# Kernel tuning notes

Hardware: AMD Instinct MI355X
Metric: run time of the kernel (lower is better)

The kernel has to match this reference:

```python
import jax, jax.numpy as jnp
import numpy as np
import math

D = 1024      # d_model
K = 64        # k_eigenstates
H = 4         # n_heads
KH = K // H   # eigenstates per head
MLP = 4 * D
B, T = 4, 4096


def setup_inputs() -> dict:
    key = jax.random.key(0)
    ks = jax.random.split(key, 16)
    rn = lambda k, shape, s: (jax.random.normal(k, shape, jnp.float32) * s)
    inp = {
        "x": rn(ks[0], (B, T, D), 1.0),
        "W_in": rn(ks[1], (2 * K, D), 1.0 / math.sqrt(D)),
        "log_decay": jax.random.uniform(ks[2], (K,), jnp.float32, -3.0, -0.1),
        "frequency": jnp.linspace(0.0, 2 * math.pi * (1 - 1.0 / K), K, dtype=jnp.float32),
        "W_sel": rn(ks[3], (2 * K, D), 0.01 / math.sqrt(D)),
        "b_sel": jnp.zeros((2 * K,), jnp.float32),
        "R": jnp.eye(KH, dtype=jnp.float32)[None] + 0.01 * rn(ks[4], (H, KH, KH), 1.0 / math.sqrt(KH)),
        "W_out": rn(ks[5], (D, 2 * K), 1.0 / math.sqrt(2 * K)),
        "W_g": rn(ks[6], (D, D), 1.0 / math.sqrt(D)),
        "b_g": jnp.full((D,), -2.0, jnp.float32),
        "g1": jnp.ones((D,), jnp.float32),
        "be1": jnp.zeros((D,), jnp.float32),
        "g2": jnp.ones((D,), jnp.float32),
        "be2": jnp.zeros((D,), jnp.float32),
        "W1": rn(ks[7], (MLP, D), 1.0 / math.sqrt(D)),
        "b1": jnp.zeros((MLP,), jnp.float32),
        "W2": rn(ks[8], (D, MLP), 1.0 / math.sqrt(MLP)),
        "b2": jnp.zeros((D,), jnp.float32),
    }
    return inp


def _ln(x, g, b):
    m = jnp.mean(x, axis=-1, keepdims=True)
    v = jnp.mean(jnp.square(x - m), axis=-1, keepdims=True)
    return (x - m) * jax.lax.rsqrt(v + 1e-5) * g + b


def _scan_combine(e1, e2):
    a1, b1 = e1
    a2, b2 = e2
    return a1 * a2, a2 * b1 + b2


def reference(x, W_in, log_decay, frequency, W_sel, b_sel, R, W_out, W_g, b_g,
              g1, be1, g2, be2, W1, b1, W2, b2):
    Bsz, Ts, Dm = x.shape
    residual = x
    x_norm = _ln(x, g1, be1)

    beta = x_norm @ W_in.T                      # [B,T,2K]
    beta_r, beta_i = jnp.split(beta, 2, axis=-1)

    delta = x_norm @ W_sel.T + b_sel            # selective modulation
    d_dec, d_fr = jnp.split(delta, 2, axis=-1)
    mag = jax.nn.sigmoid(log_decay + 0.1 * jnp.tanh(d_dec))   # [B,T,K]
    freq = frequency + 0.05 * jnp.tanh(d_fr)

    a = jax.lax.complex(mag * jnp.cos(freq), mag * jnp.sin(freq))  # lambda_t
    bc = jax.lax.complex(beta_r, beta_i)
    # inclusive prefix scan of c_t = a_t * c_{t-1} + b_t
    _, c = jax.lax.associative_scan(_scan_combine, (a, bc), axis=1)
    c_r, c_i = c.real, c.imag                   # [B,T,K]

    nH, Kh = R.shape[0], R.shape[1]
    c_r = jnp.einsum('hjk,bthk->bthj', R, c_r.reshape(Bsz, Ts, nH, Kh)).reshape(Bsz, Ts, -1)
    c_i = jnp.einsum('hjk,bthk->bthj', R, c_i.reshape(Bsz, Ts, nH, Kh)).reshape(Bsz, Ts, -1)

    h = jnp.concatenate([c_r, c_i], axis=-1) @ W_out.T
    gate = jax.nn.sigmoid(x_norm @ W_g.T + b_g)
    x = residual + gate * h

    x2 = _ln(x, g2, be2)
    x = x + (jax.nn.silu(x2 @ W1.T + b1) @ W2.T + b2)
    return x
```

## Files before the change

kernel.cpp:

```cpp
#include <hip/hip_runtime.h>
#include <math.h>

typedef __bf16 bf16_t;
typedef __attribute__((ext_vector_type(8))) __bf16 bf16x8;
typedef __attribute__((ext_vector_type(4))) float f32x4;

#define DMODEL 1024
#define NROWS  16384
#define SEQLEN 4096

static __device__ __forceinline__ float sigmoidf_(float v) { return 1.f / (1.f + __expf(-v)); }

#define GLOAD16(gsrc, ldst) __builtin_amdgcn_global_load_lds(                     \
    (const __attribute__((address_space(1))) void*)(gsrc),                        \
    (__attribute__((address_space(3))) void*)(ldst), 16, 0, 0)

__global__ __launch_bounds__(256) void ln_fused_kernel(const float* __restrict__ x,
                                                       const float* __restrict__ g,
                                                       const float* __restrict__ b,
                                                       bf16_t* __restrict__ out) {
  int row = blockIdx.x;
  int tid = threadIdx.x;
  const float4* xr = (const float4*)(x + (size_t)row * DMODEL);
  float4 v = xr[tid];
  float s  = v.x + v.y + v.z + v.w;
  float s2 = v.x*v.x + v.y*v.y + v.z*v.z + v.w*v.w;
  #pragma unroll
  for (int off = 32; off > 0; off >>= 1) {
    s  += __shfl_down(s, off);
    s2 += __shfl_down(s2, off);
  }
  __shared__ float sh[4], sh2[4];
  int lane = tid & 63, wid = tid >> 6;
  if (lane == 0) { sh[wid] = s; sh2[wid] = s2; }
  __syncthreads();
  s  = sh[0] + sh[1] + sh[2] + sh[3];
  s2 = sh2[0] + sh2[1] + sh2[2] + sh2[3];
  float m = s * (1.f / DMODEL);
  float var = fmaxf(s2 * (1.f / DMODEL) - m * m, 0.f);
  float rs = rsqrtf(var + 1e-5f);
  float4 gv = *(const float4*)&g[tid * 4];
  float4 bv = *(const float4*)&b[tid * 4];
  union { bf16_t h[4]; float2 f2; } u;
  u.h[0] = (bf16_t)((v.x - m) * rs * gv.x + bv.x);
  u.h[1] = (bf16_t)((v.y - m) * rs * gv.y + bv.y);
  u.h[2] = (bf16_t)((v.z - m) * rs * gv.z + bv.z);
  u.h[3] = (bf16_t)((v.w - m) * rs * gv.w + bv.w);
  *(float2*)&out[(size_t)row * DMODEL + tid * 4] = u.f2;
}

__global__ __launch_bounds__(256) void f32_to_bf16_kernel(const float* __restrict__ in,
                                                          bf16_t* __restrict__ out, int n) {
  int idx = (blockIdx.x * 256 + threadIdx.x) * 4;
  if (idx >= n) return;
  float4 v = *(const float4*)&in[idx];
  union { bf16_t h[4]; float2 f2; } u;
  u.h[0] = (bf16_t)v.x; u.h[1] = (bf16_t)v.y; u.h[2] = (bf16_t)v.z; u.h[3] = (bf16_t)v.w;
  *(float2*)&out[idx] = u.f2;
}

template<int EPI>
__global__ __launch_bounds__(512, 4) void gemmB_kernel(
    const bf16_t* __restrict__ A, int lda,
    const bf16_t* __restrict__ B, int ldb, int K, int nx,
    const float* __restrict__ bias,
    const float* __restrict__ res,
    const bf16_t* __restrict__ auxb,
    float* __restrict__ outf, bf16_t* __restrict__ outb, int ldout) {
  __shared__ __align__(128) bf16_t Asm[128 * 64];
  __shared__ __align__(128) bf16_t Bsm[256 * 64];
  const int nwg = gridDim.x;
  const int bid = blockIdx.x;
  const int lid = (bid & 7) * (nwg >> 3) + (bid >> 3);
  const int n0 = (lid % nx) * 256;
  const int r0 = (lid / nx) * 128;

  const int tid = threadIdx.x;
  const int lane = tid & 63;
  const int w = tid >> 6;
  const int wr = w >> 2, wc = w & 3;
  const int fr = lane & 15;
  const int q16 = (lane >> 4) * 16;
  const int swz = (fr & 7) << 4;
  const int trow = tid >> 3;
  const int scolb = ((tid & 7) ^ (trow & 7)) << 4;

  const size_t lda_b = (size_t)lda * 2;
  const size_t ldb_b = (size_t)ldb * 2;
  const char* Ab = (const char*)A;
  const char* Bb = (const char*)B;
  char* lA = (char*)Asm;
  char* lB = (char*)Bsm;

  f32x4 acc[4][4];
  #pragma unroll
  for (int m = 0; m < 4; ++m)
    #pragma unroll
    for (int n = 0; n < 4; ++n) acc[m][n] = (f32x4){0.f, 0.f, 0.f, 0.f};

  for (int kt = 0; kt < K; kt += 64) {
    const char* sa = Ab + (size_t)(r0 + trow) * lda_b + kt * 2 + scolb;
    GLOAD16(sa, lA + tid * 16);
    GLOAD16(sa + 64 * lda_b, lA + 8192 + tid * 16);
    const char* sb = Bb + (size_t)(n0 + trow) * ldb_b + kt * 2 + scolb;
    GLOAD16(sb, lB + tid * 16);
    GLOAD16(sb + 64 * ldb_b,  lB + 8192  + tid * 16);
    GLOAD16(sb + 128 * ldb_b, lB + 16384 + tid * 16);
    GLOAD16(sb + 192 * ldb_b, lB + 24576 + tid * 16);
    __syncthreads();
    #pragma unroll
    for (int kh = 0; kh < 2; ++kh) {
      bf16x8 af[4], bv[4];
      #pragma unroll
      for (int m = 0; m < 4; ++m)
        af[m] = *(const bf16x8*)(lA + (wr * 64 + m * 16 + fr) * 128 + ((kh * 64 + q16) ^ swz));
      #pragma unroll
      for (int n = 0; n < 4; ++n)
        bv[n] = *(const bf16x8*)(lB + (wc * 64 + n * 16 + fr) * 128 + ((kh * 64 + q16) ^ swz));
      #pragma unroll
      for (int m = 0; m < 4; ++m)
        #pragma unroll
        for (int n = 0; n < 4; ++n)
          acc[m][n] = __builtin_amdgcn_mfma_f32_16x16x32_bf16(af[m], bv[n], acc[m][n], 0, 0, 0);
    }
    __syncthreads();
  }

  const int rbase = (lane >> 4) * 4;
  #pragma unroll
  for (int mf = 0; mf < 4; ++mf) {
    #pragma unroll
    for (int n = 0; n < 4; ++n) {
      int row = r0 + wr * 64 + mf * 16 + rbase;
      int col = n0 + wc * 64 + n * 16 + fr;
      f32x4 v = acc[mf][n];
      #pragma unroll
      for (int j = 0; j < 4; ++j) {
        int r = row + j;
        float val = v[j];
        if (EPI == 0) {
          outf[(size_t)r * ldout + col] = val;
        } else if (EPI == 1) {
          float t2 = val + bias[col];
          t2 = t2 * sigmoidf_(t2);
          outb[(size_t)r * ldout + col] = (bf16_t)t2;
        } else if (EPI == 2) {
          outf[(size_t)r * ldout + col] = res[(size_t)r * 1024 + col] + bias[col] + val;
        } else if (EPI == 3) {
          outf[(size_t)r * ldout + col] += val;
        } else if (EPI == 4) {
          size_t idx = (size_t)r * 1024 + col;
          outf[idx] = res[idx] + sigmoidf_(val + bias[col]) * (float)auxb[idx];
        } else {
          outb[(size_t)r * ldout + col] = (bf16_t)val;
        }
      }
    }
  }
}

template<int EPI>
__global__ __launch_bounds__(256) void gemm_bf16_kernel(
    const bf16_t* __restrict__ A, int lda,
    const bf16_t* __restrict__ B, int ldb, int K, int nx,
    float* __restrict__ outf, int ldout) {
  __shared__ __align__(16) bf16_t As[128 * 32];
  __shared__ __align__(16) bf16_t Bs[128 * 32];
  const int nwg = gridDim.x;
  const int bid = blockIdx.x;
  const int lid = (bid & 7) * (nwg >> 3) + (bid >> 3);
  const int n0 = (lid % nx) * 128;
  const int r0 = (lid / nx) * 128;

  const int tid = threadIdx.x;
  const int lane = tid & 63;
  const int w = tid >> 6;
  const int wr = w >> 1, wc = w & 1;
  const int srow0 = tid >> 2;
  const int srow1 = 64 + (tid >> 2);
  const int skk = (tid & 3) * 8;
  const int fr = lane & 15;
  const int ko = (lane >> 4) * 8;

  f32x4 acc[4][4];
  #pragma unroll
  for (int m = 0; m < 4; ++m)
    #pragma unroll
    for (int n = 0; n < 4; ++n) acc[m][n] = (f32x4){0.f, 0.f, 0.f, 0.f};

  for (int k0 = 0; k0 < K; k0 += 32) {
    GLOAD16(A + (size_t)(r0 + srow0) * lda + k0 + skk, (char*)As + w * 1024);
    GLOAD16(A + (size_t)(r0 + srow1) * lda + k0 + skk, (char*)As + 4096 + w * 1024);
    GLOAD16(B + (size_t)(n0 + srow0) * ldb + k0 + skk, (char*)Bs + w * 1024);
    GLOAD16(B + (size_t)(n0 + srow1) * ldb + k0 + skk, (char*)Bs + 4096 + w * 1024);
    __syncthreads();
    bf16x8 af[4], bfr[4];
    #pragma unroll
    for (int m = 0; m < 4; ++m)
      af[m] = *(const bf16x8*)&As[(wr * 64 + m * 16 + fr) * 32 + ko];
    #pragma unroll
    for (int n = 0; n < 4; ++n)
      bfr[n] = *(const bf16x8*)&Bs[(wc * 64 + n * 16 + fr) * 32 + ko];
    #pragma unroll
    for (int m = 0; m < 4; ++m)
      #pragma unroll
      for (int n = 0; n < 4; ++n)
        acc[m][n] = __builtin_amdgcn_mfma_f32_16x16x32_bf16(af[m], bfr[n], acc[m][n], 0, 0, 0);
    __syncthreads();
  }

  const int rbase = (lane >> 4) * 4;
  #pragma unroll
  for (int m = 0; m < 4; ++m) {
    #pragma unroll
    for (int n = 0; n < 4; ++n) {
      int row = r0 + wr * 64 + m * 16 + rbase;
      int col = n0 + wc * 64 + n * 16 + fr;
      f32x4 v = acc[m][n];
      #pragma unroll
      for (int j = 0; j < 4; ++j)
        outf[(size_t)(row + j) * ldout + col] = v[j];
    }
  }
}

__global__ __launch_bounds__(256) void ew_ab_kernel(
    const float* __restrict__ bd, const float* __restrict__ b_sel,
    const float* __restrict__ log_decay, const float* __restrict__ frequency,
    float* __restrict__ a_r, float* __restrict__ a_i,
    float* __restrict__ b_r, float* __restrict__ b_i) {
  __shared__ float T[32][257];
  int bb = blockIdx.x >> 7;
  int t0 = (blockIdx.x & 127) << 5;
  int tid = threadIdx.x;
  #pragma unroll
  for (int p = 0; p < 32; ++p) {
    int idx = tid + p * 256;
    int tt = idx >> 8, j = idx & 255;
    T[tt][j] = bd[((size_t)bb * 4096 + t0 + tt) * 256 + j];
  }
  __syncthreads();
  #pragma unroll
  for (int p = 0; p < 8; ++p) {
    int idx = tid + p * 256;
    int tt = idx & 31, k = idx >> 5;
    float br_ = T[tt][k];
    float bi_ = T[tt][64 + k];
    float dd = T[tt][128 + k] + b_sel[k];
    float df = T[tt][192 + k] + b_sel[64 + k];
    float mag = sigmoidf_(log_decay[k] + 0.1f * tanhf(dd));
    float fr = frequency[k] + 0.05f * tanhf(df);
    float ar_ = mag * cosf(fr), ai_ = mag * sinf(fr);
    size_t o = ((size_t)bb * 64 + k) * 4096 + t0 + tt;
    a_r[o] = ar_; a_i[o] = ai_; b_r[o] = br_; b_i[o] = bi_;
  }
}

__global__ __launch_bounds__(256) void scan_kernel(
    const float* __restrict__ a_r, const float* __restrict__ a_i,
    const float* b_r, const float* b_i,
    float* c_r, float* c_i) {
  int seq = blockIdx.x;
  size_t base = (size_t)seq * SEQLEN;
  int tid = threadIdx.x;
  int t0 = tid * 16;
  float Ar = 1.f, Ai = 0.f, Br = 0.f, Bi = 0.f;
  #pragma unroll
  for (int s = 0; s < 16; ++s) {
    size_t t = base + t0 + s;
    float ar = a_r[t], ai = a_i[t], br = b_r[t], bi = b_i[t];
    float nBr = ar * Br - ai * Bi + br;
    float nBi = ar * Bi + ai * Br + bi;
    Br = nBr; Bi = nBi;
    float nAr = ar * Ar - ai * Ai;
    float nAi = ar * Ai + ai * Ar;
    Ar = nAr; Ai = nAi;
  }
  __shared__ float sAr[256], sAi[256], sBr[256], sBi[256];
  sAr[tid] = Ar; sAi[tid] = Ai; sBr[tid] = Br; sBi[tid] = Bi;
  for (int off = 1; off < 256; off <<= 1) {
    __syncthreads();
    float pAr = 0.f, pAi = 0.f, pBr = 0.f, pBi = 0.f;
    if (tid >= off) { pAr = sAr[tid - off]; pAi = sAi[tid - off]; pBr = sBr[tid - off]; pBi = sBi[tid - off]; }
    __syncthreads();
    if (tid >= off) {
      float cAr = sAr[tid], cAi = sAi[tid], cBr = sBr[tid], cBi = sBi[tid];
      float nBr = cAr * pBr - cAi * pBi + cBr;
      float nBi = cAr * pBi + cAi * pBr + cBi;
      float nAr = cAr * pAr - cAi * pAi;
      float nAi = cAr * pAi + cAi * pAr;
      sAr[tid] = nAr; sAi[tid] = nAi; sBr[tid] = nBr; sBi[tid] = nBi;
    }
  }
  __syncthreads();
  float cr = (tid > 0) ? sBr[tid - 1] : 0.f;
  float ci = (tid > 0) ? sBi[tid - 1] : 0.f;
  #pragma unroll
  for (int s = 0; s < 16; ++s) {
    size_t t = base + t0 + s;
    float ar = a_r[t], ai = a_i[t], br = b_r[t], bi = b_i[t];
    float nr = ar * cr - ai * ci + br;
    float ni = ar * ci + ai * cr + bi;
    cr = nr; ci = ni;
    c_r[t] = cr; c_i[t] = ci;
  }
}

__global__ __launch_bounds__(256) void transpose_cc_kernel(
    const float* __restrict__ c_r, const float* __restrict__ c_i,
    bf16_t* __restrict__ cc) {
  __shared__ float Tr[64][65];
  __shared__ float Ti[64][65];
  int t0 = blockIdx.x * 64;
  int bb = blockIdx.y;
  int tid = threadIdx.x;
  int tt = tid & 63;
  int q = tid >> 6;
  #pragma unroll
  for (int p = 0; p < 16; ++p) {
    int k = p * 4 + q;
    size_t src = ((size_t)bb * 64 + k) * 4096 + t0 + tt;
    Tr[tt][k] = c_r[src];
    Ti[tt][k] = c_i[src];
  }
  __syncthreads();
  #pragma unroll
  for (int p = 0; p < 16; ++p) {
    int tt2 = p * 4 + q;
    int k = tid & 63;
    size_t row = (size_t)bb * 4096 + t0 + tt2;
    cc[row * 128 + k] = (bf16_t)Tr[tt2][k];
    cc[row * 128 + 64 + k] = (bf16_t)Ti[tt2][k];
  }
}

__global__ __launch_bounds__(256) void weff_kernel(const float* __restrict__ W_out,
                                                   const float* __restrict__ R,
                                                   bf16_t* __restrict__ Weff) {
  int idx = blockIdx.x * 256 + threadIdx.x;
  int d = idx >> 7, col = idx & 127;
  int k = col & 63, h = k >> 4, kk = k & 15;
  int off = (col < 64) ? 0 : 64;
  float s = 0.f;
  #pragma unroll
  for (int j = 0; j < 16; ++j)
    s += W_out[d * 128 + off + h * 16 + j] * R[h * 256 + j * 16 + kk];
  Weff[idx] = (bf16_t)s;
}

extern "C" void kernel_launch(void* const* d_in, const int* in_sizes, int n_in,
                              void* d_out, int out_size, void* d_ws, size_t ws_size,
                              hipStream_t stream) {
  (void)in_sizes; (void)n_in; (void)out_size;
  const float* x         = (const float*)d_in[0];
  const float* W_in      = (const float*)d_in[1];
  const float* log_decay = (const float*)d_in[2];
  const float* frequency = (const float*)d_in[3];
  const float* W_sel     = (const float*)d_in[4];
  const float* b_sel     = (const float*)d_in[5];
  const float* R         = (const float*)d_in[6];
  const float* W_out     = (const float*)d_in[7];
  const float* W_g       = (const float*)d_in[8];
  const float* b_g       = (const float*)d_in[9];
  const float* g1        = (const float*)d_in[10];
  const float* be1       = (const float*)d_in[11];
  const float* g2        = (const float*)d_in[12];
  const float* be2       = (const float*)d_in[13];
  const float* W1        = (const float*)d_in[14];
  const float* b1        = (const float*)d_in[15];
  const float* W2        = (const float*)d_in[16];
  const float* b2        = (const float*)d_in[17];
  float* out = (float*)d_out;
  float* ws  = (float*)d_ws;

  const size_t M1 = (size_t)1 << 20;
  const bool full = ws_size >= (size_t)62 * M1 * sizeof(float);

  float* bd   = ws;
  float* xmid = ws;
  float* a_r  = ws + 16 * M1;
  float* a_i  = ws + 20 * M1;
  float* b_rr = ws + 24 * M1;
  float* b_ii = ws + 28 * M1;
  bf16_t* hbufb = (bf16_t*)(ws + 16 * M1);
  bf16_t* mid = (bf16_t*)(ws + 16 * M1);
  size_t wx = full ? 48 * M1 : 32 * M1;
  size_t wc_off = full ? 56 * M1 : 40 * M1;
  size_t wb = full ? 57 * M1 : 41 * M1;
  bf16_t* xn  = (bf16_t*)(ws + wx);
  bf16_t* cc  = (bf16_t*)(ws + wc_off);
  bf16_t* Wbd = (bf16_t*)(ws + wb);
  bf16_t* Wgb = (bf16_t*)(ws + wb + (128 << 10));
  bf16_t* W1b = (bf16_t*)(ws + wb + (640 << 10));
  bf16_t* W2b = (bf16_t*)(ws + wb + 2 * M1 + (640 << 10));
  bf16_t* Wef = (bf16_t*)(ws + wb + 4 * M1 + (640 << 10));

  dim3 blk(256);
  dim3 blk512(512);

  ln_fused_kernel<<<NROWS, blk, 0, stream>>>(x, g1, be1, xn);

  f32_to_bf16_kernel<<<128, blk, 0, stream>>>(W_in, Wbd, 128 * 1024);
  f32_to_bf16_kernel<<<128, blk, 0, stream>>>(W_sel, Wbd + 128 * 1024, 128 * 1024);
  f32_to_bf16_kernel<<<1024, blk, 0, stream>>>(W_g, Wgb, 1024 * 1024);
  f32_to_bf16_kernel<<<4096, blk, 0, stream>>>(W1, W1b, 4 * 1024 * 1024);
  f32_to_bf16_kernel<<<4096, blk, 0, stream>>>(W2, W2b, 4 * 1024 * 1024);
  weff_kernel<<<512, blk, 0, stream>>>(W_out, R, Wef);

  gemm_bf16_kernel<0><<<256, blk, 0, stream>>>(xn, 1024, Wbd, 1024, 1024, 2, bd, 256);

  ew_ab_kernel<<<512, blk, 0, stream>>>(bd, b_sel, log_decay, frequency, a_r, a_i, b_rr, b_ii);
  scan_kernel<<<256, blk, 0, stream>>>(a_r, a_i, b_rr, b_ii, b_rr, b_ii);
  transpose_cc_kernel<<<dim3(64, 4), blk, 0, stream>>>(b_rr, b_ii, cc);

  gemmB_kernel<5><<<512, blk512, 0, stream>>>(
      cc, 128, Wef, 128, 128, 4, nullptr, nullptr, nullptr, nullptr, hbufb, 1024);

  gemmB_kernel<4><<<512, blk512, 0, stream>>>(
      xn, 1024, Wgb, 1024, 1024, 4, b_g, x, hbufb, xmid, nullptr, 1024);

  ln_fused_kernel<<<NROWS, blk, 0, stream>>>(xmid, g2, be2, xn);

  if (full) {
    gemmB_kernel<1><<<2048, blk512, 0, stream>>>(
        xn, 1024, W1b, 1024, 1024, 16, b1, nullptr, nullptr, nullptr, mid, 4096);
    gemmB_kernel<2><<<512, blk512, 0, stream>>>(
        mid, 4096, W2b, 4096, 4096, 4, b2, xmid, nullptr, out, nullptr, 1024);
  } else {
    for (int h = 0; h < 2; ++h) {
      gemmB_kernel<1><<<1024, blk512, 0, stream>>>(
          xn, 1024, W1b + (size_t)h * 2048 * 1024, 1024, 1024, 8,
          b1 + h * 2048, nullptr, nullptr, nullptr, mid, 2048);
      if (h == 0) {
        gemmB_kernel<2><<<512, blk512, 0, stream>>>(
            mid, 2048, W2b, 4096, 2048, 4, b2, xmid, nullptr, out, nullptr, 1024);
      } else {
        gemmB_kernel<3><<<512, blk512, 0, stream>>>(
            mid, 2048, W2b + 2048, 4096, 2048, 4, nullptr, nullptr, nullptr, out, nullptr, 1024);
      }
    }
  }
}
```

Before: 476.7 us.

## Double-buffer LDS in main GEMM with 32-wide K tiles

Replaces the single-buffered 64-wide K-tile loop in the main bf16 GEMM with a double-buffered loop over 32-wide K tiles. The next tile's global-to-LDS load is issued before computing on the current one, which removes one barrier per iteration and overlaps memory with MFMA work. The XOR swizzle is dropped because each LDS row is now 64 bytes, which may bring back bank conflicts on the fragment reads. Each iteration also has half as many MFMAs to hide latency behind.

```diff
diff --git a/kernel.cpp b/kernel.cpp
--- a/kernel.cpp
+++ b/kernel.cpp
@@ -60,15 +60,14 @@
 }
 
 template<int EPI>
-__global__ __launch_bounds__(512, 4) void gemmB_kernel(
+__global__ __launch_bounds__(512, 4) void gemmC_kernel(
     const bf16_t* __restrict__ A, int lda,
     const bf16_t* __restrict__ B, int ldb, int K, int nx,
     const float* __restrict__ bias,
     const float* __restrict__ res,
     const bf16_t* __restrict__ auxb,
     float* __restrict__ outf, bf16_t* __restrict__ outb, int ldout) {
-  __shared__ __align__(128) bf16_t Asm[128 * 64];
-  __shared__ __align__(128) bf16_t Bsm[256 * 64];
+  __shared__ __align__(128) char ldsp[49152];
   const int nwg = gridDim.x;
   const int bid = blockIdx.x;
   const int lid = (bid & 7) * (nwg >> 3) + (bid >> 3);
@@ -81,16 +80,13 @@
   const int wr = w >> 2, wc = w & 3;
   const int fr = lane & 15;
   const int q16 = (lane >> 4) * 16;
-  const int swz = (fr & 7) << 4;
-  const int trow = tid >> 3;
-  const int scolb = ((tid & 7) ^ (trow & 7)) << 4;
+  const int tr4 = tid >> 2;
+  const int sl = (tid & 3) * 16;
 
   const size_t lda_b = (size_t)lda * 2;
   const size_t ldb_b = (size_t)ldb * 2;
   const char* Ab = (const char*)A;
   const char* Bb = (const char*)B;
-  char* lA = (char*)Asm;
-  char* lB = (char*)Bsm;
 
   f32x4 acc[4][4];
   #pragma unroll
@@ -98,32 +94,37 @@
     #pragma unroll
     for (int n = 0; n < 4; ++n) acc[m][n] = (f32x4){0.f, 0.f, 0.f, 0.f};
 
-  for (int kt = 0; kt < K; kt += 64) {
-    const char* sa = Ab + (size_t)(r0 + trow) * lda_b + kt * 2 + scolb;
-    GLOAD16(sa, lA + tid * 16);
-    GLOAD16(sa + 64 * lda_b, lA + 8192 + tid * 16);
-    const char* sb = Bb + (size_t)(n0 + trow) * ldb_b + kt * 2 + scolb;
-    GLOAD16(sb, lB + tid * 16);
-    GLOAD16(sb + 64 * ldb_b,  lB + 8192  + tid * 16);
-    GLOAD16(sb + 128 * ldb_b, lB + 16384 + tid * 16);
-    GLOAD16(sb + 192 * ldb_b, lB + 24576 + tid * 16);
-    __syncthreads();
-    #pragma unroll
-    for (int kh = 0; kh < 2; ++kh) {
-      bf16x8 af[4], bv[4];
-      #pragma unroll
-      for (int m = 0; m < 4; ++m)
-        af[m] = *(const bf16x8*)(lA + (wr * 64 + m * 16 + fr) * 128 + ((kh * 64 + q16) ^ swz));
+  auto stage = [&](int d, int kt) {
+    const char* sa = Ab + (size_t)(r0 + tr4) * lda_b + kt * 2 + sl;
+    GLOAD16(sa, ldsp + d * 8192 + tid * 16);
+    const char* sb = Bb + (size_t)(n0 + tr4) * ldb_b + kt * 2 + sl;
+    GLOAD16(sb, ldsp + 16384 + d * 16384 + tid * 16);
+    GLOAD16(sb + 128 * ldb_b, ldsp + 16384 + d * 16384 + 8192 + tid * 16);
+  };
+  auto compute = [&](int d) {
+    bf16x8 af[4], bv[4];
+    #pragma unroll
+    for (int m = 0; m < 4; ++m)
+      af[m] = *(const bf16x8*)(ldsp + d * 8192 + (wr * 64 + m * 16 + fr) * 64 + q16);
+    #pragma unroll
+    for (int n = 0; n < 4; ++n)
+      bv[n] = *(const bf16x8*)(ldsp + 16384 + d * 16384 + (wc * 64 + n * 16 + fr) * 64 + q16);
+    #pragma unroll
+    for (int m = 0; m < 4; ++m)
       #pragma unroll
       for (int n = 0; n < 4; ++n)
-        bv[n] = *(const bf16x8*)(lB + (wc * 64 + n * 16 + fr) * 128 + ((kh * 64 + q16) ^ swz));
-      #pragma unroll
-      for (int m = 0; m < 4; ++m)
-        #pragma unroll
-        for (int n = 0; n < 4; ++n)
-          acc[m][n] = __builtin_amdgcn_mfma_f32_16x16x32_bf16(af[m], bv[n], acc[m][n], 0, 0, 0);
-    }
+        acc[m][n] = __builtin_amdgcn_mfma_f32_16x16x32_bf16(af[m], bv[n], acc[m][n], 0, 0, 0);
+  };
+
+  const int nt = K >> 5;
+  stage(0, 0);
+  __syncthreads();
+  int d = 0;
+  for (int t = 0; t < nt; ++t) {
+    if (t + 1 < nt) stage(d ^ 1, (t + 1) << 5);
+    compute(d);
     __syncthreads();
+    d ^= 1;
   }
 
   const int rbase = (lane >> 4) * 4;
@@ -413,29 +414,29 @@
   scan_kernel<<<256, blk, 0, stream>>>(a_r, a_i, b_rr, b_ii, b_rr, b_ii);
   transpose_cc_kernel<<<dim3(64, 4), blk, 0, stream>>>(b_rr, b_ii, cc);
 
-  gemmB_kernel<5><<<512, blk512, 0, stream>>>(
+  gemmC_kernel<5><<<512, blk512, 0, stream>>>(
       cc, 128, Wef, 128, 128, 4, nullptr, nullptr, nullptr, nullptr, hbufb, 1024);
 
-  gemmB_kernel<4><<<512, blk512, 0, stream>>>(
+  gemmC_kernel<4><<<512, blk512, 0, stream>>>(
       xn, 1024, Wgb, 1024, 1024, 4, b_g, x, hbufb, xmid, nullptr, 1024);
 
   ln_fused_kernel<<<NROWS, blk, 0, stream>>>(xmid, g2, be2, xn);
 
   if (full) {
-    gemmB_kernel<1><<<2048, blk512, 0, stream>>>(
+    gemmC_kernel<1><<<2048, blk512, 0, stream>>>(
         xn, 1024, W1b, 1024, 1024, 16, b1, nullptr, nullptr, nullptr, mid, 4096);
-    gemmB_kernel<2><<<512, blk512, 0, stream>>>(
+    gemmC_kernel<2><<<512, blk512, 0, stream>>>(
         mid, 4096, W2b, 4096, 4096, 4, b2, xmid, nullptr, out, nullptr, 1024);
   } else {
     for (int h = 0; h < 2; ++h) {
-      gemmB_kernel<1><<<1024, blk512, 0, stream>>>(
+      gemmC_kernel<1><<<1024, blk512, 0, stream>>>(
           xn, 1024, W1b + (size_t)h * 2048 * 1024, 1024, 1024, 8,
           b1 + h * 2048, nullptr, nullptr, nullptr, mid, 2048);
       if (h == 0) {
-        gemmB_kernel<2><<<512, blk512, 0, stream>>>(
+        gemmC_kernel<2><<<512, blk512, 0, stream>>>(
             mid, 2048, W2b, 4096, 2048, 4, b2, xmid, nullptr, out, nullptr, 1024);
       } else {
-        gemmB_kernel<3><<<512, blk512, 0, stream>>>(
+        gemmC_kernel<3><<<512, blk512, 0, stream>>>(
             mid, 2048, W2b + 2048, 4096, 2048, 4, nullptr, nullptr, nullptr, out, nullptr, 1024);
       }
     }
```

After: 517.5 us. +8.6%, slower.

## Replace 512-thread GEMM with 256-thread 256x128 tile, K-step 32 kernel

Applied to the files above, without the earlier changes.

Swaps the main bf16 MFMA GEMM for a variant using 256 threads, a 256x128 output tile (rows x cols), and a 32-wide K step with a 24KB shared buffer and a new XOR swizzle. Each wave now computes a 128x64 sub-tile with 8x4 accumulators, loading each A fragment once per m and reusing the B fragments across all m. The aim is higher register-level reuse and smaller LDS use so more workgroups fit per CU. In exchange there are twice as many K iterations and barriers, and more accumulator registers per thread.

```diff
diff --git a/kernel.cpp b/kernel.cpp
--- a/kernel.cpp
+++ b/kernel.cpp
@@ -60,78 +60,71 @@
 }
 
 template<int EPI>
-__global__ __launch_bounds__(512, 4) void gemmB_kernel(
+__global__ __launch_bounds__(256, 3) void gemmD_kernel(
     const bf16_t* __restrict__ A, int lda,
     const bf16_t* __restrict__ B, int ldb, int K, int nx,
     const float* __restrict__ bias,
     const float* __restrict__ res,
     const bf16_t* __restrict__ auxb,
     float* __restrict__ outf, bf16_t* __restrict__ outb, int ldout) {
-  __shared__ __align__(128) bf16_t Asm[128 * 64];
-  __shared__ __align__(128) bf16_t Bsm[256 * 64];
+  __shared__ __align__(128) char ldsp[24576];
   const int nwg = gridDim.x;
   const int bid = blockIdx.x;
   const int lid = (bid & 7) * (nwg >> 3) + (bid >> 3);
-  const int n0 = (lid % nx) * 256;
-  const int r0 = (lid / nx) * 128;
+  const int n0 = (lid % nx) * 128;
+  const int r0 = (lid / nx) * 256;
 
   const int tid = threadIdx.x;
   const int lane = tid & 63;
   const int w = tid >> 6;
-  const int wr = w >> 2, wc = w & 3;
+  const int wr = w >> 1, wc = w & 1;
   const int fr = lane & 15;
   const int q16 = (lane >> 4) * 16;
-  const int swz = (fr & 7) << 4;
-  const int trow = tid >> 3;
-  const int scolb = ((tid & 7) ^ (trow & 7)) << 4;
+  const int rdcol = q16 ^ (((fr >> 1) & 3) << 4);
+  const int trow = tid >> 2;
+  const int scolb = (((tid & 3) ^ ((trow >> 1) & 3)) << 4);
 
   const size_t lda_b = (size_t)lda * 2;
   const size_t ldb_b = (size_t)ldb * 2;
   const char* Ab = (const char*)A;
   const char* Bb = (const char*)B;
-  char* lA = (char*)Asm;
-  char* lB = (char*)Bsm;
-
-  f32x4 acc[4][4];
-  #pragma unroll
-  for (int m = 0; m < 4; ++m)
+
+  f32x4 acc[8][4];
+  #pragma unroll
+  for (int m = 0; m < 8; ++m)
     #pragma unroll
     for (int n = 0; n < 4; ++n) acc[m][n] = (f32x4){0.f, 0.f, 0.f, 0.f};
 
-  for (int kt = 0; kt < K; kt += 64) {
+  for (int kt = 0; kt < K; kt += 32) {
     const char* sa = Ab + (size_t)(r0 + trow) * lda_b + kt * 2 + scolb;
-    GLOAD16(sa, lA + tid * 16);
-    GLOAD16(sa + 64 * lda_b, lA + 8192 + tid * 16);
+    GLOAD16(sa,               ldsp +         tid * 16);
+    GLOAD16(sa +  64 * lda_b, ldsp +  4096 + tid * 16);
+    GLOAD16(sa + 128 * lda_b, ldsp +  8192 + tid * 16);
+    GLOAD16(sa + 192 * lda_b, ldsp + 12288 + tid * 16);
     const char* sb = Bb + (size_t)(n0 + trow) * ldb_b + kt * 2 + scolb;
-    GLOAD16(sb, lB + tid * 16);
-    GLOAD16(sb + 64 * ldb_b,  lB + 8192  + tid * 16);
-    GLOAD16(sb + 128 * ldb_b, lB + 16384 + tid * 16);
-    GLOAD16(sb + 192 * ldb_b, lB + 24576 + tid * 16);
-    __syncthreads();
-    #pragma unroll
-    for (int kh = 0; kh < 2; ++kh) {
-      bf16x8 af[4], bv[4];
-      #pragma unroll
-      for (int m = 0; m < 4; ++m)
-        af[m] = *(const bf16x8*)(lA + (wr * 64 + m * 16 + fr) * 128 + ((kh * 64 + q16) ^ swz));
+    GLOAD16(sb,               ldsp + 16384 + tid * 16);
+    GLOAD16(sb +  64 * ldb_b, ldsp + 20480 + tid * 16);
+    __syncthreads();
+    bf16x8 bv[4];
+    #pragma unroll
+    for (int n = 0; n < 4; ++n)
+      bv[n] = *(const bf16x8*)(ldsp + 16384 + (wc * 64 + n * 16 + fr) * 64 + rdcol);
+    #pragma unroll
+    for (int m = 0; m < 8; ++m) {
+      bf16x8 af = *(const bf16x8*)(ldsp + (wr * 128 + m * 16 + fr) * 64 + rdcol);
       #pragma unroll
       for (int n = 0; n < 4; ++n)
-        bv[n] = *(const bf16x8*)(lB + (wc * 64 + n * 16 + fr) * 128 + ((kh * 64 + q16) ^ swz));
-      #pragma unroll
-      for (int m = 0; m < 4; ++m)
-        #pragma unroll
-        for (int n = 0; n < 4; ++n)
-          acc[m][n] = __builtin_amdgcn_mfma_f32_16x16x32_bf16(af[m], bv[n], acc[m][n], 0, 0, 0);
+        acc[m][n] = __builtin_amdgcn_mfma_f32_16x16x32_bf16(af, bv[n], acc[m][n], 0, 0, 0);
     }
     __syncthreads();
   }
 
   const int rbase = (lane >> 4) * 4;
   #pragma unroll
-  for (int mf = 0; mf < 4; ++mf) {
+  for (int mf = 0; mf < 8; ++mf) {
     #pragma unroll
     for (int n = 0; n < 4; ++n) {
-      int row = r0 + wr * 64 + mf * 16 + rbase;
+      int row = r0 + wr * 128 + mf * 16 + rbase;
       int col = n0 + wc * 64 + n * 16 + fr;
       f32x4 v = acc[mf][n];
       #pragma unroll
@@ -396,7 +389,6 @@
   bf16_t* Wef = (bf16_t*)(ws + wb + 4 * M1 + (640 << 10));
 
   dim3 blk(256);
-  dim3 blk512(512);
 
   ln_fused_kernel<<<NROWS, blk, 0, stream>>>(x, g1, be1, xn);
 
@@ -413,30 +405,30 @@
   scan_kernel<<<256, blk, 0, stream>>>(a_r, a_i, b_rr, b_ii, b_rr, b_ii);
   transpose_cc_kernel<<<dim3(64, 4), blk, 0, stream>>>(b_rr, b_ii, cc);
 
-  gemmB_kernel<5><<<512, blk512, 0, stream>>>(
-      cc, 128, Wef, 128, 128, 4, nullptr, nullptr, nullptr, nullptr, hbufb, 1024);
-
-  gemmB_kernel<4><<<512, blk512, 0, stream>>>(
-      xn, 1024, Wgb, 1024, 1024, 4, b_g, x, hbufb, xmid, nullptr, 1024);
+  gemmD_kernel<5><<<512, blk, 0, stream>>>(
+      cc, 128, Wef, 128, 128, 8, nullptr, nullptr, nullptr, nullptr, hbufb, 1024);
+
+  gemmD_kernel<4><<<512, blk, 0, stream>>>(
+      xn, 1024, Wgb, 1024, 1024, 8, b_g, x, hbufb, xmid, nullptr, 1024);
 
   ln_fused_kernel<<<NROWS, blk, 0, stream>>>(xmid, g2, be2, xn);
 
   if (full) {
-    gemmB_kernel<1><<<2048, blk512, 0, stream>>>(
-        xn, 1024, W1b, 1024, 1024, 16, b1, nullptr, nullptr, nullptr, mid, 4096);
-    gemmB_kernel<2><<<512, blk512, 0, stream>>>(
-        mid, 4096, W2b, 4096, 4096, 4, b2, xmid, nullptr, out, nullptr, 1024);
+    gemmD_kernel<1><<<2048, blk, 0, stream>>>(
+        xn, 1024, W1b, 1024, 1024, 32, b1, nullptr, nullptr, nullptr, mid, 4096);
+    gemmD_kernel<2><<<512, blk, 0, stream>>>(
+        mid, 4096, W2b, 4096, 4096, 8, b2, xmid, nullptr, out, nullptr, 1024);
   } else {
     for (int h = 0; h < 2; ++h) {
-      gemmB_kernel<1><<<1024, blk512, 0, stream>>>(
-          xn, 1024, W1b + (size_t)h * 2048 * 1024, 1024, 1024, 8,
+      gemmD_kernel<1><<<1024, blk, 0, stream>>>(
+          xn, 1024, W1b + (size_t)h * 2048 * 1024, 1024, 1024, 16,
           b1 + h * 2048, nullptr, nullptr, nullptr, mid, 2048);
       if (h == 0) {
-        gemmB_kernel<2><<<512, blk512, 0, stream>>>(
-            mid, 2048, W2b, 4096, 2048, 4, b2, xmid, nullptr, out, nullptr, 1024);
+        gemmD_kernel<2><<<512, blk, 0, stream>>>(
+            mid, 2048, W2b, 4096, 2048, 8, b2, xmid, nullptr, out, nullptr, 1024);
       } else {
-        gemmB_kernel<3><<<512, blk512, 0, stream>>>(
-            mid, 2048, W2b + 2048, 4096, 2048, 4, nullptr, nullptr, nullptr, out, nullptr, 1024);
+        gemmD_kernel<3><<<512, blk, 0, stream>>>(
+            mid, 2048, W2b + 2048, 4096, 2048, 8, nullptr, nullptr, nullptr, out, nullptr, 1024);
       }
     }
   }
```

Result: slower. 575.3 us (+20.7%).

## Fuse gate computation into scan, transpose beta GEMM, store residual stream in bf16

Applied to the files above, without the earlier changes.

The element-wise decay/frequency kernel is merged into the scan kernel. The projection GEMM is swapped to emit a transposed [256 x 16384] layout so the scan reads contiguous per-channel vectors, and it computes gates with fast tanh/sincos. The intermediate residual xmid is now stored as bf16, with a new bf16-input LayerNorm, to cut memory traffic in the second half. This removes the a/b round-trip buffers and one launch, at the cost of lower precision in the residual carried to the final output.

```diff
diff --git a/kernel.cpp b/kernel.cpp
--- a/kernel.cpp
+++ b/kernel.cpp
@@ -3,6 +3,7 @@
 
 typedef __bf16 bf16_t;
 typedef __attribute__((ext_vector_type(8))) __bf16 bf16x8;
+typedef __attribute__((ext_vector_type(4))) __bf16 bf16x4;
 typedef __attribute__((ext_vector_type(4))) float f32x4;
 
 #define DMODEL 1024
@@ -10,6 +11,11 @@
 #define SEQLEN 4096
 
 static __device__ __forceinline__ float sigmoidf_(float v) { return 1.f / (1.f + __expf(-v)); }
+static __device__ __forceinline__ float tanhf_(float v) {
+  v = fminf(fmaxf(v, -15.f), 15.f);
+  float e = __expf(-2.f * v);
+  return (1.f - e) / (1.f + e);
+}
 
 #define GLOAD16(gsrc, ldst) __builtin_amdgcn_global_load_lds(                     \
     (const __attribute__((address_space(1))) void*)(gsrc),                        \
@@ -49,6 +55,40 @@
   *(float2*)&out[(size_t)row * DMODEL + tid * 4] = u.f2;
 }
 
+__global__ __launch_bounds__(256) void ln_fused_bf16_kernel(const bf16_t* __restrict__ x,
+                                                            const float* __restrict__ g,
+                                                            const float* __restrict__ b,
+                                                            bf16_t* __restrict__ out) {
+  int row = blockIdx.x;
+  int tid = threadIdx.x;
+  bf16x4 hv = *(const bf16x4*)(x + (size_t)row * DMODEL + tid * 4);
+  float v0 = (float)hv[0], v1 = (float)hv[1], v2 = (float)hv[2], v3 = (float)hv[3];
+  float s  = v0 + v1 + v2 + v3;
+  float s2 = v0*v0 + v1*v1 + v2*v2 + v3*v3;
+  #pragma unroll
+  for (int off = 32; off > 0; off >>= 1) {
+    s  += __shfl_down(s, off);
+    s2 += __shfl_down(s2, off);
+  }
+  __shared__ float sh[4], sh2[4];
+  int lane = tid & 63, wid = tid >> 6;
+  if (lane == 0) { sh[wid] = s; sh2[wid] = s2; }
+  __syncthreads();
+  s  = sh[0] + sh[1] + sh[2] + sh[3];
+  s2 = sh2[0] + sh2[1] + sh2[2] + sh2[3];
+  float m = s * (1.f / DMODEL);
+  float var = fmaxf(s2 * (1.f / DMODEL) - m * m, 0.f);
+  float rs = rsqrtf(var + 1e-5f);
+  float4 gv = *(const float4*)&g[tid * 4];
+  float4 bv = *(const float4*)&b[tid * 4];
+  union { bf16_t h[4]; float2 f2; } u;
+  u.h[0] = (bf16_t)((v0 - m) * rs * gv.x + bv.x);
+  u.h[1] = (bf16_t)((v1 - m) * rs * gv.y + bv.y);
+  u.h[2] = (bf16_t)((v2 - m) * rs * gv.z + bv.z);
+  u.h[3] = (bf16_t)((v3 - m) * rs * gv.w + bv.w);
+  *(float2*)&out[(size_t)row * DMODEL + tid * 4] = u.f2;
+}
+
 __global__ __launch_bounds__(256) void f32_to_bf16_kernel(const float* __restrict__ in,
                                                           bf16_t* __restrict__ out, int n) {
   int idx = (blockIdx.x * 256 + threadIdx.x) * 4;
@@ -64,7 +104,8 @@
     const bf16_t* __restrict__ A, int lda,
     const bf16_t* __restrict__ B, int ldb, int K, int nx,
     const float* __restrict__ bias,
-    const float* __restrict__ res,
+    const float* __restrict__ resf,
+    const bf16_t* __restrict__ resb,
     const bf16_t* __restrict__ auxb,
     float* __restrict__ outf, bf16_t* __restrict__ outb, int ldout) {
   __shared__ __align__(128) bf16_t Asm[128 * 64];
@@ -145,12 +186,13 @@
           t2 = t2 * sigmoidf_(t2);
           outb[(size_t)r * ldout + col] = (bf16_t)t2;
         } else if (EPI == 2) {
-          outf[(size_t)r * ldout + col] = res[(size_t)r * 1024 + col] + bias[col] + val;
+          outf[(size_t)r * ldout + col] =
+              (float)resb[(size_t)r * 1024 + col] + bias[col] + val;
         } else if (EPI == 3) {
           outf[(size_t)r * ldout + col] += val;
         } else if (EPI == 4) {
           size_t idx = (size_t)r * 1024 + col;
-          outf[idx] = res[idx] + sigmoidf_(val + bias[col]) * (float)auxb[idx];
+          outb[idx] = (bf16_t)(resf[idx] + sigmoidf_(val + bias[col]) * (float)auxb[idx]);
         } else {
           outb[(size_t)r * ldout + col] = (bf16_t)val;
         }
@@ -224,58 +266,46 @@
   }
 }
 
-__global__ __launch_bounds__(256) void ew_ab_kernel(
-    const float* __restrict__ bd, const float* __restrict__ b_sel,
+__global__ __launch_bounds__(256) void scan_fused_kernel(
+    const float* __restrict__ bdt,
     const float* __restrict__ log_decay, const float* __restrict__ frequency,
-    float* __restrict__ a_r, float* __restrict__ a_i,
-    float* __restrict__ b_r, float* __restrict__ b_i) {
-  __shared__ float T[32][257];
-  int bb = blockIdx.x >> 7;
-  int t0 = (blockIdx.x & 127) << 5;
+    const float* __restrict__ b_sel,
+    float* __restrict__ c_r, float* __restrict__ c_i) {
+  int seq = blockIdx.x;
+  int bb = seq >> 6, k = seq & 63;
   int tid = threadIdx.x;
-  #pragma unroll
-  for (int p = 0; p < 32; ++p) {
-    int idx = tid + p * 256;
-    int tt = idx >> 8, j = idx & 255;
-    T[tt][j] = bd[((size_t)bb * 4096 + t0 + tt) * 256 + j];
-  }
-  __syncthreads();
-  #pragma unroll
-  for (int p = 0; p < 8; ++p) {
-    int idx = tid + p * 256;
-    int tt = idx & 31, k = idx >> 5;
-    float br_ = T[tt][k];
-    float bi_ = T[tt][64 + k];
-    float dd = T[tt][128 + k] + b_sel[k];
-    float df = T[tt][192 + k] + b_sel[64 + k];
-    float mag = sigmoidf_(log_decay[k] + 0.1f * tanhf(dd));
-    float fr = frequency[k] + 0.05f * tanhf(df);
-    float ar_ = mag * cosf(fr), ai_ = mag * sinf(fr);
-    size_t o = ((size_t)bb * 64 + k) * 4096 + t0 + tt;
-    a_r[o] = ar_; a_i[o] = ai_; b_r[o] = br_; b_i[o] = bi_;
-  }
-}
-
-__global__ __launch_bounds__(256) void scan_kernel(
-    const float* __restrict__ a_r, const float* __restrict__ a_i,
-    const float* b_r, const float* b_i,
-    float* c_r, float* c_i) {
-  int seq = blockIdx.x;
-  size_t base = (size_t)seq * SEQLEN;
-  int tid = threadIdx.x;
-  int t0 = tid * 16;
+  size_t col = (size_t)bb * 4096 + tid * 16;
+  const f32x4* pbr = (const f32x4*)(bdt + (size_t)k * 16384 + col);
+  const f32x4* pbi = (const f32x4*)(bdt + (size_t)(64 + k) * 16384 + col);
+  const f32x4* pdd = (const f32x4*)(bdt + (size_t)(128 + k) * 16384 + col);
+  const f32x4* pdf = (const f32x4*)(bdt + (size_t)(192 + k) * 16384 + col);
+  const float ld = log_decay[k], fq = frequency[k];
+  const float bsd = b_sel[k], bsf = b_sel[64 + k];
+
+  float arv[16], aiv[16], brv[16], biv[16];
   float Ar = 1.f, Ai = 0.f, Br = 0.f, Bi = 0.f;
   #pragma unroll
-  for (int s = 0; s < 16; ++s) {
-    size_t t = base + t0 + s;
-    float ar = a_r[t], ai = a_i[t], br = b_r[t], bi = b_i[t];
-    float nBr = ar * Br - ai * Bi + br;
-    float nBi = ar * Bi + ai * Br + bi;
-    Br = nBr; Bi = nBi;
-    float nAr = ar * Ar - ai * Ai;
-    float nAi = ar * Ai + ai * Ar;
-    Ar = nAr; Ai = nAi;
-  }
+  for (int g = 0; g < 4; ++g) {
+    f32x4 vbr = pbr[g], vbi = pbi[g], vdd = pdd[g], vdf = pdf[g];
+    #pragma unroll
+    for (int j = 0; j < 4; ++j) {
+      int s = g * 4 + j;
+      float mag = sigmoidf_(ld + 0.1f * tanhf_(vdd[j] + bsd));
+      float f = fq + 0.05f * tanhf_(vdf[j] + bsf);
+      float sn, cs;
+      __sincosf(f, &sn, &cs);
+      float ar = mag * cs, ai = mag * sn;
+      float br = vbr[j], bi = vbi[j];
+      arv[s] = ar; aiv[s] = ai; brv[s] = br; biv[s] = bi;
+      float nBr = ar * Br - ai * Bi + br;
+      float nBi = ar * Bi + ai * Br + bi;
+      Br = nBr; Bi = nBi;
+      float nAr = ar * Ar - ai * Ai;
+      float nAi = ar * Ai + ai * Ar;
+      Ar = nAr; Ai = nAi;
+    }
+  }
+
   __shared__ float sAr[256], sAi[256], sBr[256], sBi[256];
   sAr[tid] = Ar; sAi[tid] = Ai; sBr[tid] = Br; sBi[tid] = Bi;
   for (int off = 1; off < 256; off <<= 1) {
@@ -295,14 +325,22 @@
   __syncthreads();
   float cr = (tid > 0) ? sBr[tid - 1] : 0.f;
   float ci = (tid > 0) ? sBi[tid - 1] : 0.f;
-  #pragma unroll
-  for (int s = 0; s < 16; ++s) {
-    size_t t = base + t0 + s;
-    float ar = a_r[t], ai = a_i[t], br = b_r[t], bi = b_i[t];
-    float nr = ar * cr - ai * ci + br;
-    float ni = ar * ci + ai * cr + bi;
-    cr = nr; ci = ni;
-    c_r[t] = cr; c_i[t] = ci;
+
+  float* outr = c_r + (size_t)seq * 4096 + tid * 16;
+  float* outi = c_i + (size_t)seq * 4096 + tid * 16;
+  #pragma unroll
+  for (int g = 0; g < 4; ++g) {
+    f32x4 vr, vi;
+    #pragma unroll
+    for (int j = 0; j < 4; ++j) {
+      int s = g * 4 + j;
+      float nr = arv[s] * cr - aiv[s] * ci + brv[s];
+      float ni = arv[s] * ci + aiv[s] * cr + biv[s];
+      cr = nr; ci = ni;
+      vr[j] = cr; vi[j] = ci;
+    }
+    *(f32x4*)(outr + g * 4) = vr;
+    *(f32x4*)(outi + g * 4) = vi;
   }
 }
 
@@ -374,21 +412,18 @@
   float* ws  = (float*)d_ws;
 
   const size_t M1 = (size_t)1 << 20;
-  const bool full = ws_size >= (size_t)62 * M1 * sizeof(float);
-
-  float* bd   = ws;
-  float* xmid = ws;
-  float* a_r  = ws + 16 * M1;
-  float* a_i  = ws + 20 * M1;
-  float* b_rr = ws + 24 * M1;
-  float* b_ii = ws + 28 * M1;
-  bf16_t* hbufb = (bf16_t*)(ws + 16 * M1);
-  bf16_t* mid = (bf16_t*)(ws + 16 * M1);
-  size_t wx = full ? 48 * M1 : 32 * M1;
-  size_t wc_off = full ? 56 * M1 : 40 * M1;
-  size_t wb = full ? 57 * M1 : 41 * M1;
-  bf16_t* xn  = (bf16_t*)(ws + wx);
-  bf16_t* cc  = (bf16_t*)(ws + wc_off);
+  const bool full = ws_size >= (size_t)61 * M1 * sizeof(float);
+
+  float* bd_t = ws;
+  float* c_r  = ws + 4 * M1;
+  float* c_i  = ws + 8 * M1;
+  bf16_t* cc  = (bf16_t*)(ws + 12 * M1);
+  bf16_t* mid = (bf16_t*)ws;
+  size_t o = full ? 32 * M1 : 16 * M1;
+  bf16_t* xmid  = (bf16_t*)(ws + o);
+  bf16_t* hbufb = (bf16_t*)(ws + o + 8 * M1);
+  bf16_t* xn    = (bf16_t*)(ws + o + 16 * M1);
+  size_t wb = o + 24 * M1;
   bf16_t* Wbd = (bf16_t*)(ws + wb);
   bf16_t* Wgb = (bf16_t*)(ws + wb + (128 << 10));
   bf16_t* W1b = (bf16_t*)(ws + wb + (640 << 10));
@@ -407,36 +442,36 @@
   f32_to_bf16_kernel<<<4096, blk, 0, stream>>>(W2, W2b, 4 * 1024 * 1024);
   weff_kernel<<<512, blk, 0, stream>>>(W_out, R, Wef);
 
-  gemm_bf16_kernel<0><<<256, blk, 0, stream>>>(xn, 1024, Wbd, 1024, 1024, 2, bd, 256);
-
-  ew_ab_kernel<<<512, blk, 0, stream>>>(bd, b_sel, log_decay, frequency, a_r, a_i, b_rr, b_ii);
-  scan_kernel<<<256, blk, 0, stream>>>(a_r, a_i, b_rr, b_ii, b_rr, b_ii);
-  transpose_cc_kernel<<<dim3(64, 4), blk, 0, stream>>>(b_rr, b_ii, cc);
+  gemm_bf16_kernel<0><<<256, blk, 0, stream>>>(Wbd, 1024, xn, 1024, 1024, 128, bd_t, 16384);
+
+  scan_fused_kernel<<<256, blk, 0, stream>>>(bd_t, log_decay, frequency, b_sel, c_r, c_i);
+
+  transpose_cc_kernel<<<dim3(64, 4), blk, 0, stream>>>(c_r, c_i, cc);
 
   gemmB_kernel<5><<<512, blk512, 0, stream>>>(
-      cc, 128, Wef, 128, 128, 4, nullptr, nullptr, nullptr, nullptr, hbufb, 1024);
+      cc, 128, Wef, 128, 128, 4, nullptr, nullptr, nullptr, nullptr, nullptr, hbufb, 1024);
 
   gemmB_kernel<4><<<512, blk512, 0, stream>>>(
-      xn, 1024, Wgb, 1024, 1024, 4, b_g, x, hbufb, xmid, nullptr, 1024);
-
-  ln_fused_kernel<<<NROWS, blk, 0, stream>>>(xmid, g2, be2, xn);
+      xn, 1024, Wgb, 1024, 1024, 4, b_g, x, nullptr, hbufb, nullptr, xmid, 1024);
+
+  ln_fused_bf16_kernel<<<NROWS, blk, 0, stream>>>(xmid, g2, be2, xn);
 
   if (full) {
     gemmB_kernel<1><<<2048, blk512, 0, stream>>>(
-        xn, 1024, W1b, 1024, 1024, 16, b1, nullptr, nullptr, nullptr, mid, 4096);
+        xn, 1024, W1b, 1024, 1024, 16, b1, nullptr, nullptr, nullptr, nullptr, mid, 4096);
     gemmB_kernel<2><<<512, blk512, 0, stream>>>(
-        mid, 4096, W2b, 4096, 4096, 4, b2, xmid, nullptr, out, nullptr, 1024);
+        mid, 4096, W2b, 4096, 4096, 4, b2, nullptr, xmid, nullptr, out, nullptr, 1024);
   } else {
     for (int h = 0; h < 2; ++h) {
       gemmB_kernel<1><<<1024, blk512, 0, stream>>>(
           xn, 1024, W1b + (size_t)h * 2048 * 1024, 1024, 1024, 8,
-          b1 + h * 2048, nullptr, nullptr, nullptr, mid, 2048);
+          b1 + h * 2048, nullptr, nullptr, nullptr, nullptr, mid, 2048);
       if (h == 0) {
         gemmB_kernel<2><<<512, blk512, 0, stream>>>(
-            mid, 2048, W2b, 4096, 2048, 4, b2, xmid, nullptr, out, nullptr, 1024);
+            mid, 2048, W2b, 4096, 2048, 4, b2, nullptr, xmid, nullptr, out, nullptr, 1024);
       } else {
         gemmB_kernel<3><<<512, blk512, 0, stream>>>(
-            mid, 2048, W2b + 2048, 4096, 2048, 4, nullptr, nullptr, nullptr, out, nullptr, 1024);
+            mid, 2048, W2b + 2048, 4096, 2048, 4, nullptr, nullptr, nullptr, nullptr, out, nullptr, 1024);
       }
     }
   }
```

New measurement: 446.2 us (median of 2 runs). 6.4% less time.
